# Kernel optimization log

Hardware: AMD Instinct MI355X
Metric: run time of the kernel (lower is better)

The kernel has to match this reference:

```python
import jax, jax.numpy as jnp
import numpy as np

IGNORE_INDEX = 0


def _lovasz_softmax(inputs, targets):
    # inputs: [B, C, H, W] logits; targets: [B, H, W] int class ids
    C = inputs.shape[1]
    probs = jax.nn.softmax(inputs, axis=1)                      # [B,C,H,W]
    probs_flat = probs.transpose(0, 2, 3, 1).reshape(-1, C)     # [P,C]
    t = targets.reshape(-1)                                     # [P]
    valid = (t != IGNORE_INDEX)                                 # [P] bool

    # Per-class foreground indicator, zeroed at invalid pixels: [C,P]
    fg = ((t[None, :] == jnp.arange(C)[:, None]) & valid[None, :]).astype(probs_flat.dtype)
    # Errors |fg - prob|; invalid pixels forced to error 0 so they sort to the
    # end and contribute nothing (equivalent to filtering them out, since both
    # their error and the causal cumsums at earlier positions are unaffected).
    errors = jnp.abs(fg - probs_flat.T) * valid[None, :].astype(probs_flat.dtype)  # [C,P]

    # Sort each class's errors descending; permutation is non-differentiable (constant).
    order = jnp.argsort(-errors, axis=1)                        # [C,P]
    errors_sorted = jnp.take_along_axis(errors, order, axis=1)
    fg_sorted = jnp.take_along_axis(fg, order, axis=1)

    # Lovasz gradient (Alg. 1), vectorized over classes.
    gts = fg_sorted.sum(axis=1, keepdims=True)                  # [C,1]
    intersection = gts - jnp.cumsum(fg_sorted, axis=1)
    union = gts + jnp.cumsum(1.0 - fg_sorted, axis=1)
    jaccard = 1.0 - intersection / union                        # [C,P]
    grad = jnp.concatenate([jaccard[:, :1], jaccard[:, 1:] - jaccard[:, :-1]], axis=1)

    per_class = jnp.sum(jax.nn.relu(errors_sorted) * jax.lax.stop_gradient(grad), axis=1)  # [C]

    # classes='present': only classes with foreground among valid pixels, skip ignore_index.
    present = (fg.sum(axis=1) > 0) & (jnp.arange(C) != IGNORE_INDEX)  # [C] bool
    n_present = jnp.sum(present.astype(per_class.dtype))
    total = jnp.sum(jnp.where(present, per_class, 0.0))
    return jnp.where(n_present > 0, total / jnp.maximum(n_present, 1.0), 0.0)


def setup_inputs() -> dict:
    key = jax.random.key(0)
    k1, k2 = jax.random.split(key)
    B, C, H, W = 8, 8, 512, 512
    inputs = jax.random.normal(k1, (B, C, H, W), dtype=jnp.float32)
    targets = jax.random.randint(k2, (B, H, W), 0, C, dtype=jnp.int32)
    return {"inputs": inputs, "targets": targets}


def reference(inputs, targets):
    return _lovasz_softmax(inputs, targets)
```

## Files before the change

### kernel.cpp

```cpp
#include <hip/hip_runtime.h>
#include <stdint.h>

#define HW      262144
#define NCLASS  8
#define PIX     2097152
#define NCLS    7
#define KB      512
#define BLOCK   256
#define CHUNK   4096
#define NBLK    (PIX / CHUNK)
#define HSZ     (NCLS * KB)

#define OFF_TS   28672
#define ZERO_BYTES 28688

__global__ __launch_bounds__(BLOCK) void lovasz_hist_kernel(
    const float* __restrict__ logits, const int* __restrict__ targets,
    unsigned long long* __restrict__ gNF)
{
    __shared__ unsigned int sPacked[HSZ];

    const int tid = threadIdx.x;
    for (int i = tid; i < HSZ; i += BLOCK) sPacked[i] = 0u;
    __syncthreads();

    const int base_p = blockIdx.x * CHUNK;
    #pragma unroll 1
    for (int it = 0; it < CHUNK / BLOCK; ++it) {
        const int p = base_p + it * BLOCK + tid;
        const int t = targets[p];
        if (t != 0) {
            const int b  = p >> 18;
            const int hw = p & (HW - 1);
            const float* xp = logits + (size_t)b * (NCLASS * HW) + hw;
            float x[NCLASS];
            #pragma unroll
            for (int c = 0; c < NCLASS; ++c) x[c] = xp[c * HW];

            float m = x[0];
            #pragma unroll
            for (int c = 1; c < NCLASS; ++c) m = fmaxf(m, x[c]);
            float ex[NCLASS];
            float s = 0.0f;
            #pragma unroll
            for (int c = 0; c < NCLASS; ++c) { ex[c] = __expf(x[c] - m); s += ex[c]; }
            const float inv = 1.0f / s;

            #pragma unroll
            for (int c = 1; c < NCLASS; ++c) {
                const float pc = ex[c] * inv;
                const bool  fg = (t == c);
                const float err = fg ? (1.0f - pc) : pc;
                int k = (int)(err * (float)KB);
                k = (k > KB - 1) ? (KB - 1) : k;
                atomicAdd(&sPacked[(c - 1) * KB + k], fg ? 0x10001u : 1u);
            }
        }
    }
    __syncthreads();

    for (int i = tid; i < HSZ; i += BLOCK) {
        const unsigned pk = sPacked[i];
        if (pk) {
            const unsigned long long v =
                ((unsigned long long)(pk >> 16) << 32) | (unsigned long long)(pk & 0xFFFFu);
            atomicAdd(&gNF[i], v);
        }
    }
}

__global__ __launch_bounds__(256) void lovasz_scan_kernel(
    const unsigned long long* __restrict__ gNF,
    float* __restrict__ totalSum, unsigned int* __restrict__ totalCnt,
    unsigned int* __restrict__ done, float* __restrict__ out)
{
    const int c = blockIdx.x;
    const int tid = threadIdx.x;
    const unsigned long long* NF = gNF + c * KB;

    unsigned int n[2], f[2];
    unsigned long long tnf = 0ull;
    #pragma unroll
    for (int j = 0; j < 2; ++j) {
        const int k = KB - 1 - (tid * 2 + j);
        const unsigned long long v = NF[k];
        n[j] = (unsigned)(v & 0xFFFFFFFFull);
        f[j] = (unsigned)(v >> 32);
        tnf += (unsigned long long)n[j] | ((unsigned long long)f[j] << 32);
    }

    __shared__ unsigned long long buf[2][256];
    int cur = 0;
    buf[0][tid] = tnf;
    __syncthreads();
    for (int off = 1; off < 256; off <<= 1) {
        unsigned long long v = buf[cur][tid];
        if (tid >= off) v += buf[cur][tid - off];
        buf[cur ^ 1][tid] = v;
        __syncthreads();
        cur ^= 1;
    }
    const unsigned long long inc = buf[cur][tid];
    const unsigned int G = (unsigned)(buf[cur][255] >> 32);

    double contrib = 0.0;
    if (G > 0) {
        long long i0 = (long long)(unsigned)(inc & 0xFFFFFFFFull) - n[0] - n[1];
        long long F0 = (long long)(unsigned)(inc >> 32) - f[0] - f[1];
        const long long Gl = (long long)G;
        #pragma unroll
        for (int j = 0; j < 2; ++j) {
            if (n[j]) {
                const long long i1 = i0 + n[j];
                const long long F1 = F0 + f[j];
                const long long num = (Gl - F0) * (Gl + i1 - F1)
                                    - (Gl - F1) * (Gl + i0 - F0);
                const double den = (double)(Gl + i0 - F0) * (double)(Gl + i1 - F1);
                const double dJ = (double)num / den;
                const double e = ((double)(KB - 1 - (tid * 2 + j)) + 0.5) / (double)KB;
                contrib += e * dJ;
            }
            i0 += n[j]; F0 += f[j];
        }
    }

    __shared__ double red[256];
    red[tid] = contrib;
    __syncthreads();
    for (int off = 128; off > 0; off >>= 1) {
        if (tid < off) red[tid] += red[tid + off];
        __syncthreads();
    }

    if (tid == 0) {
        if (G > 0) {
            atomicAdd(totalSum, (float)red[0]);
            atomicAdd(totalCnt, 1u);
        }
        __threadfence();
        const unsigned old = atomicAdd(done, 1u);
        if (old == NCLS - 1) {
            __threadfence();
            const float ts = atomicAdd(totalSum, 0.0f);
            const unsigned cnt = atomicAdd(totalCnt, 0u);
            out[0] = (cnt > 0) ? (ts / (float)cnt) : 0.0f;
        }
    }
}

extern "C" void kernel_launch(void* const* d_in, const int* in_sizes, int n_in,
                              void* d_out, int out_size, void* d_ws, size_t ws_size,
                              hipStream_t stream) {
    const float* logits  = (const float*)d_in[0];
    const int*   targets = (const int*)d_in[1];
    float* out = (float*)d_out;

    uint8_t* ws = (uint8_t*)d_ws;
    unsigned long long* gNF = (unsigned long long*)ws;
    float*        totalSum  = (float*)(ws + OFF_TS);
    unsigned int* totalCnt  = (unsigned int*)(ws + OFF_TS + 4);
    unsigned int* done      = (unsigned int*)(ws + OFF_TS + 8);

    hipMemsetAsync(ws, 0, ZERO_BYTES, stream);

    lovasz_hist_kernel<<<NBLK, BLOCK, 0, stream>>>(logits, targets, gNF);
    lovasz_scan_kernel<<<NCLS, 256, 0, stream>>>(gNF, totalSum, totalCnt, done, out);
}
```

Baseline: 120.7 us.

## Fuse histogram and scan into one kernel with last-block finalization and vectorized loads

```diff
diff --git a/kernel.cpp b/kernel.cpp
--- a/kernel.cpp
+++ b/kernel.cpp
@@ -6,46 +6,59 @@
 #define PIX     2097152
 #define NCLS    7
 #define KB      512
-#define BLOCK   256
+#define BLOCK   1024
 #define CHUNK   4096
 #define NBLK    (PIX / CHUNK)
 #define HSZ     (NCLS * KB)
 
-#define OFF_TS   28672
-#define ZERO_BYTES 28688
+#define OFF_DONE   28672
+#define ZERO_BYTES 28680
 
-__global__ __launch_bounds__(BLOCK) void lovasz_hist_kernel(
+__global__ __launch_bounds__(BLOCK, 8) void lovasz_fused_kernel(
     const float* __restrict__ logits, const int* __restrict__ targets,
-    unsigned long long* __restrict__ gNF)
+    unsigned long long* __restrict__ gNF, unsigned int* __restrict__ done,
+    float* __restrict__ out)
 {
-    __shared__ unsigned int sPacked[HSZ];
+    __shared__ unsigned long long smem[1792];
+    __shared__ int    sIsLast;
+    __shared__ double sC[NCLS];
+    __shared__ unsigned int sGv[NCLS];
 
+    unsigned int* sPacked = (unsigned int*)smem;
     const int tid = threadIdx.x;
+
     for (int i = tid; i < HSZ; i += BLOCK) sPacked[i] = 0u;
     __syncthreads();
 
-    const int base_p = blockIdx.x * CHUNK;
-    #pragma unroll 1
-    for (int it = 0; it < CHUNK / BLOCK; ++it) {
-        const int p = base_p + it * BLOCK + tid;
-        const int t = targets[p];
+    const int p0 = blockIdx.x * CHUNK + tid * 4;
+    const int b  = p0 >> 18;
+    const int hw = p0 & (HW - 1);
+    const float* xp = logits + (size_t)b * (NCLASS * HW) + hw;
+
+    const int4 t4 = *(const int4*)(targets + p0);
+    float4 x4[NCLASS];
+    #pragma unroll
+    for (int c = 0; c < NCLASS; ++c)
+        x4[c] = *(const float4*)(xp + (size_t)c * HW);
+
+    const int tarr[4] = {t4.x, t4.y, t4.z, t4.w};
+    #pragma unroll
+    for (int j = 0; j < 4; ++j) {
+        const int t = tarr[j];
+        float x[NCLASS];
+        #pragma unroll
+        for (int c = 0; c < NCLASS; ++c)
+            x[c] = (j == 0) ? x4[c].x : (j == 1) ? x4[c].y
+                 : (j == 2) ? x4[c].z : x4[c].w;
         if (t != 0) {
-            const int b  = p >> 18;
-            const int hw = p & (HW - 1);
-            const float* xp = logits + (size_t)b * (NCLASS * HW) + hw;
-            float x[NCLASS];
-            #pragma unroll
-            for (int c = 0; c < NCLASS; ++c) x[c] = xp[c * HW];
-
             float m = x[0];
             #pragma unroll
             for (int c = 1; c < NCLASS; ++c) m = fmaxf(m, x[c]);
+            float s = 0.0f;
             float ex[NCLASS];
-            float s = 0.0f;
             #pragma unroll
             for (int c = 0; c < NCLASS; ++c) { ex[c] = __expf(x[c] - m); s += ex[c]; }
             const float inv = 1.0f / s;
-
             #pragma unroll
             for (int c = 1; c < NCLASS; ++c) {
                 const float pc = ex[c] * inv;
@@ -67,84 +80,93 @@
             atomicAdd(&gNF[i], v);
         }
     }
-}
+    __syncthreads();
 
-__global__ __launch_bounds__(256) void lovasz_scan_kernel(
-    const unsigned long long* __restrict__ gNF,
-    float* __restrict__ totalSum, unsigned int* __restrict__ totalCnt,
-    unsigned int* __restrict__ done, float* __restrict__ out)
-{
-    const int c = blockIdx.x;
-    const int tid = threadIdx.x;
-    const unsigned long long* NF = gNF + c * KB;
+    if (tid == 0) {
+        __threadfence();
+        sIsLast = (atomicAdd(done, 1u) == NBLK - 1) ? 1 : 0;
+    }
+    __syncthreads();
+    if (!sIsLast) return;
 
-    unsigned int n[2], f[2];
+    const bool active = (tid < NCLS * 128);
+    const int c = tid >> 7;
+    const int s = tid & 127;
+
+    unsigned int n[4] = {0, 0, 0, 0}, f[4] = {0, 0, 0, 0};
     unsigned long long tnf = 0ull;
-    #pragma unroll
-    for (int j = 0; j < 2; ++j) {
-        const int k = KB - 1 - (tid * 2 + j);
-        const unsigned long long v = NF[k];
-        n[j] = (unsigned)(v & 0xFFFFFFFFull);
-        f[j] = (unsigned)(v >> 32);
-        tnf += (unsigned long long)n[j] | ((unsigned long long)f[j] << 32);
+    if (active) {
+        #pragma unroll
+        for (int j = 0; j < 4; ++j) {
+            const int k = KB - 1 - (s * 4 + j);
+            const unsigned long long v = atomicAdd(&gNF[c * KB + k], 0ull);
+            n[j] = (unsigned)v;
+            f[j] = (unsigned)(v >> 32);
+            tnf += v;
+        }
     }
 
-    __shared__ unsigned long long buf[2][256];
-    int cur = 0;
-    buf[0][tid] = tnf;
+    unsigned long long* src = smem;
+    unsigned long long* dst = smem + 896;
+    if (active) src[tid] = tnf;
     __syncthreads();
-    for (int off = 1; off < 256; off <<= 1) {
-        unsigned long long v = buf[cur][tid];
-        if (tid >= off) v += buf[cur][tid - off];
-        buf[cur ^ 1][tid] = v;
+    #pragma unroll
+    for (int off = 1; off < 128; off <<= 1) {
+        unsigned long long v = 0ull;
+        if (active) {
+            v = src[tid];
+            if (s >= off) v += src[tid - off];
+        }
+        if (active) dst[tid] = v;
         __syncthreads();
-        cur ^= 1;
+        unsigned long long* tmp = src; src = dst; dst = tmp;
     }
-    const unsigned long long inc = buf[cur][tid];
-    const unsigned int G = (unsigned)(buf[cur][255] >> 32);
+
+    unsigned long long inc = 0ull, segtot = 0ull;
+    if (active) {
+        inc    = src[tid];
+        segtot = src[(c << 7) | 127];
+    }
+    const unsigned int G = (unsigned)(segtot >> 32);
 
     double contrib = 0.0;
-    if (G > 0) {
-        long long i0 = (long long)(unsigned)(inc & 0xFFFFFFFFull) - n[0] - n[1];
-        long long F0 = (long long)(unsigned)(inc >> 32) - f[0] - f[1];
+    if (active && G > 0) {
+        long long i0 = (long long)(unsigned)inc        - n[0] - n[1] - n[2] - n[3];
+        long long F0 = (long long)(unsigned)(inc >> 32) - f[0] - f[1] - f[2] - f[3];
         const long long Gl = (long long)G;
         #pragma unroll
-        for (int j = 0; j < 2; ++j) {
+        for (int j = 0; j < 4; ++j) {
             if (n[j]) {
                 const long long i1 = i0 + n[j];
                 const long long F1 = F0 + f[j];
                 const long long num = (Gl - F0) * (Gl + i1 - F1)
                                     - (Gl - F1) * (Gl + i0 - F0);
                 const double den = (double)(Gl + i0 - F0) * (double)(Gl + i1 - F1);
-                const double dJ = (double)num / den;
-                const double e = ((double)(KB - 1 - (tid * 2 + j)) + 0.5) / (double)KB;
-                contrib += e * dJ;
+                const double e = ((double)(KB - 1 - (s * 4 + j)) + 0.5) / (double)KB;
+                contrib += e * ((double)num / den);
             }
             i0 += n[j]; F0 += f[j];
         }
     }
 
-    __shared__ double red[256];
-    red[tid] = contrib;
+    double* red = (double*)dst;
+    if (active) red[tid] = contrib;
     __syncthreads();
-    for (int off = 128; off > 0; off >>= 1) {
-        if (tid < off) red[tid] += red[tid + off];
+    #pragma unroll
+    for (int off = 64; off >= 1; off >>= 1) {
+        if (active && s < off) red[tid] += red[tid + off];
         __syncthreads();
     }
 
+    if (active && s == 0) { sC[c] = red[tid]; sGv[c] = G; }
+    __syncthreads();
     if (tid == 0) {
-        if (G > 0) {
-            atomicAdd(totalSum, (float)red[0]);
-            atomicAdd(totalCnt, 1u);
-        }
-        __threadfence();
-        const unsigned old = atomicAdd(done, 1u);
-        if (old == NCLS - 1) {
-            __threadfence();
-            const float ts = atomicAdd(totalSum, 0.0f);
-            const unsigned cnt = atomicAdd(totalCnt, 0u);
-            out[0] = (cnt > 0) ? (ts / (float)cnt) : 0.0f;
-        }
+        double tot = 0.0;
+        int cnt = 0;
+        #pragma unroll
+        for (int i = 0; i < NCLS; ++i)
+            if (sGv[i] > 0) { tot += sC[i]; ++cnt; }
+        out[0] = cnt ? (float)(tot / (double)cnt) : 0.0f;
     }
 }
 
@@ -157,12 +179,8 @@
 
     uint8_t* ws = (uint8_t*)d_ws;
     unsigned long long* gNF = (unsigned long long*)ws;
-    float*        totalSum  = (float*)(ws + OFF_TS);
-    unsigned int* totalCnt  = (unsigned int*)(ws + OFF_TS + 4);
-    unsigned int* done      = (unsigned int*)(ws + OFF_TS + 8);
+    unsigned int* done      = (unsigned int*)(ws + OFF_DONE);
 
     hipMemsetAsync(ws, 0, ZERO_BYTES, stream);
-
-    lovasz_hist_kernel<<<NBLK, BLOCK, 0, stream>>>(logits, targets, gNF);
-    lovasz_scan_kernel<<<NCLS, 256, 0, stream>>>(gNF, totalSum, totalCnt, done, out);
+    lovasz_fused_kernel<<<NBLK, BLOCK, 0, stream>>>(logits, targets, gNF, done, out);
 }
```

Result: no change. 122.0 us (+1.1%).
